# Performance work log

Measured on AMD Instinct MI355X. Metric: run time of the kernel, lower is better.

Reference implementation:

```python
import jax, jax.numpy as jnp
import numpy as np

B, T, C = 16, 2048, 64

def setup_inputs() -> dict:
    key = jax.random.key(0)
    x = jax.random.normal(key, (B, T, C), dtype=jnp.float32)
    # learned scalar params (as in build()): r_sigma init 0.01, margin init 0.0
    r_sigma = jnp.array([0.01], dtype=jnp.float32)
    margin = jnp.array([0.0], dtype=jnp.float32)
    return {"x": x, "r_sigma": r_sigma, "margin": margin}

def reference(x, r_sigma, margin):
    # Pairwise squared euclidean distances via the gram trick:
    # ||xi - xj||^2 = ||xi||^2 + ||xj||^2 - 2 xi.xj  (mathematically identical
    # to the original diff -> norm -> square, but avoids the (B,T,T,C) tensor
    # and the non-differentiable sqrt(0) on the diagonal).
    _, size, _ = x.shape
    sq = jnp.sum(x * x, axis=-1)                              # (B,T)
    gram = jnp.einsum('btc,bsc->bts', x, x)                   # (B,T,T)
    sqdist = jnp.maximum(sq[:, :, None] + sq[:, None, :] - 2.0 * gram, 0.0)
    # Gaussian kernel with learned inverse-bandwidth and margin
    Kmat = jnp.exp(-sqdist * r_sigma[0] + margin[0])          # (B,T,T)
    # off-diagonal mask (zero self-similarity)
    Kmat = Kmat * (1.0 - jnp.eye(size, dtype=x.dtype))
    # residual kernel attention: x + K @ x
    return x + jnp.einsum('bts,bsc->btc', Kmat, x)
```

## Files before the change

### kernel.cpp

```cpp
#include <hip/hip_runtime.h>
#include <stdint.h>
#include <stddef.h>

#define BB 16
#define TT 2048
#define CC 64

typedef __attribute__((ext_vector_type(8))) short short8;
typedef __attribute__((ext_vector_type(4))) float f32x4;

#if defined(__has_builtin)
#if __has_builtin(__builtin_amdgcn_exp2f)
#define EXP2(x) __builtin_amdgcn_exp2f(x)
#else
#define EXP2(x) exp2f(x)
#endif
#else
#define EXP2(x) exp2f(x)
#endif

static __device__ __forceinline__ unsigned short f2bf(float f) {
  union { float f; unsigned int u; } v; v.f = f;
  unsigned int u = v.u;
  return (unsigned short)((u + 0x7FFFu + ((u >> 16) & 1u)) >> 16);
}

__global__ __launch_bounds__(256) void prep_kernel(
    const float* __restrict__ x, unsigned short* __restrict__ xb,
    unsigned short* __restrict__ xbT, float* __restrict__ sq)
{
  __shared__ float tile[64][65];
  __shared__ float rs[64][4];
  const int b   = blockIdx.x >> 5;
  const int t0  = (blockIdx.x & 31) << 6;
  const int tid = threadIdx.x;
  const int r   = tid >> 2, qd = tid & 3;

  const float* src = x + ((size_t)(b * TT + t0 + r) * CC + qd * 16);
  float v[16];
  float ssq = 0.f;
#pragma unroll
  for (int k = 0; k < 4; ++k) {
    f32x4 t4 = ((const f32x4*)src)[k];
#pragma unroll
    for (int j = 0; j < 4; ++j) { float f = t4[j]; v[k * 4 + j] = f; ssq += f * f; }
  }

  unsigned short hb[16];
#pragma unroll
  for (int j = 0; j < 16; ++j) hb[j] = f2bf(v[j]);
  unsigned short* dstb = xb + ((size_t)(b * TT + t0 + r) * CC + qd * 16);
  ((short8*)dstb)[0] = *(const short8*)(hb);
  ((short8*)dstb)[1] = *(const short8*)(hb + 8);

#pragma unroll
  for (int j = 0; j < 16; ++j) tile[r][qd * 16 + j] = v[j];
  rs[r][qd] = ssq;
  __syncthreads();

  if (tid < 64)
    sq[(size_t)b * TT + t0 + tid] = rs[tid][0] + rs[tid][1] + rs[tid][2] + rs[tid][3];

  const int c = tid >> 2, tq = tid & 3;
  unsigned short ht[16];
#pragma unroll
  for (int j = 0; j < 16; ++j) ht[j] = f2bf(tile[tq * 16 + j][c]);
  unsigned short* dstT = xbT + ((size_t)(b * CC + c) * TT + t0 + tq * 16);
  ((short8*)dstT)[0] = *(const short8*)(ht);
  ((short8*)dstT)[1] = *(const short8*)(ht + 8);
}

__global__ __launch_bounds__(256, 2) void attn_kernel(
    const float* __restrict__ x, const unsigned short* __restrict__ xb,
    const unsigned short* __restrict__ xbT, const float* __restrict__ sq,
    const float* __restrict__ rsig, const float* __restrict__ marg,
    float* __restrict__ out)
{
  __shared__ unsigned short Klds[2][64 * 64];
  __shared__ unsigned short Vlds[2][64 * 64];
  __shared__ unsigned short Plds[4][16 * 64];

  const int bid = ((blockIdx.x & 7) << 6) | (blockIdx.x >> 3);
  const int b   = bid >> 5;
  const int qb  = (bid & 31) << 6;
  const int tid = threadIdx.x;
  const int w = tid >> 6, lane = tid & 63;
  const int hi = lane >> 4, lo = lane & 15;

  const float L2E = 1.44269504088896f;
  const float rl2 = -rsig[0] * L2E;
  const float ml2 = marg[0] * L2E;

  const unsigned short* xb_b  = xb  + (size_t)b * TT * CC;
  const unsigned short* xbT_b = xbT + (size_t)b * CC * TT;
  const float* sq_b = sq + (size_t)b * TT;

  const int q0 = qb + w * 16;

  short8 qf[2];
#pragma unroll
  for (int ks = 0; ks < 2; ++ks)
    qf[ks] = *(const short8*)(xb_b + (size_t)(q0 + lo) * CC + ks * 32 + hi * 8);

  float aq[4];
#pragma unroll
  for (int r = 0; r < 4; ++r) aq[r] = sq_b[q0 + hi * 4 + r];

  f32x4 oacc[4];
#pragma unroll
  for (int ct = 0; ct < 4; ++ct) oacc[ct] = (f32x4){0.f, 0.f, 0.f, 0.f};

  const int srow = tid >> 3, slot = tid & 7;
  const int swz0 = srow * 64        + ((slot ^ (srow & 7)) * 8);
  const int swz1 = (srow + 32) * 64 + ((slot ^ (srow & 7)) * 8);

  short8 stg0, stg1, stg2, stg3;

  auto LOADT = [&](int t) {
    const size_t sb = (size_t)t * 64;
    stg0 = *(const short8*)(xb_b  + (sb + srow) * CC + slot * 8);
    stg1 = *(const short8*)(xb_b  + (sb + 32 + srow) * CC + slot * 8);
    stg2 = *(const short8*)(xbT_b + (size_t)srow * TT + sb + slot * 8);
    stg3 = *(const short8*)(xbT_b + (size_t)(srow + 32) * TT + sb + slot * 8);
  };
  auto WRITET = [&](int bf) {
    *(short8*)(&Klds[bf][swz0]) = stg0;
    *(short8*)(&Klds[bf][swz1]) = stg1;
    *(short8*)(&Vlds[bf][swz0]) = stg2;
    *(short8*)(&Vlds[bf][swz1]) = stg3;
  };

  LOADT(0); WRITET(0);
  __syncthreads();

  for (int t = 0; t < 32; ++t) {
    const int cur = t & 1;
    if (t + 1 < 32) LOADT(t + 1);

    const int sb = t * 64;
    float as[4];
#pragma unroll
    for (int ct = 0; ct < 4; ++ct) as[ct] = sq_b[sb + ct * 16 + lo];

    f32x4 sac[4];
#pragma unroll
    for (int ct = 0; ct < 4; ++ct) sac[ct] = (f32x4){0.f, 0.f, 0.f, 0.f};

#pragma unroll
    for (int ct = 0; ct < 4; ++ct) {
#pragma unroll
      for (int ks = 0; ks < 2; ++ks) {
        const short8 kf = *(const short8*)(
            &Klds[cur][(ct * 16 + lo) * 64 + (((ks * 4 + hi) ^ (lo & 7)) * 8)]);
        sac[ct] = __builtin_amdgcn_mfma_f32_16x16x32_bf16(qf[ks], kf, sac[ct], 0, 0, 0);
      }
    }

    const bool dtile = (sb <= q0 + 15) && (q0 <= sb + 63);
#pragma unroll
    for (int ct = 0; ct < 4; ++ct) {
#pragma unroll
      for (int r = 0; r < 4; ++r) {
        float d = aq[r] + as[ct] - 2.f * sac[ct][r];
        d = fmaxf(d, 0.f);
        float kk = EXP2(fmaf(d, rl2, ml2));
        if (dtile && (q0 + hi * 4 + r == sb + ct * 16 + lo)) kk = 0.f;
        const int s = ct * 16 + lo, q = hi * 4 + r;
        Plds[w][q * 64 + (((s >> 3) ^ (q & 7)) * 8) + (s & 7)] = f2bf(kk);
      }
    }

    short8 pf[2];
#pragma unroll
    for (int ks = 0; ks < 2; ++ks)
      pf[ks] = *(const short8*)(
          &Plds[w][lo * 64 + (((ks * 4 + hi) ^ (lo & 7)) * 8)]);

#pragma unroll
    for (int ct = 0; ct < 4; ++ct) {
#pragma unroll
      for (int ks = 0; ks < 2; ++ks) {
        const short8 vf = *(const short8*)(
            &Vlds[cur][(ct * 16 + lo) * 64 + (((ks * 4 + hi) ^ (lo & 7)) * 8)]);
        oacc[ct] = __builtin_amdgcn_mfma_f32_16x16x32_bf16(pf[ks], vf, oacc[ct], 0, 0, 0);
      }
    }

    if (t + 1 < 32) WRITET(cur ^ 1);
    __syncthreads();
  }

#pragma unroll
  for (int ct = 0; ct < 4; ++ct) {
#pragma unroll
    for (int r = 0; r < 4; ++r) {
      const int q = q0 + hi * 4 + r;
      const int c = ct * 16 + lo;
      const size_t idx = (size_t)(b * TT + q) * CC + c;
      out[idx] = x[idx] + oacc[ct][r];
    }
  }
}

extern "C" void kernel_launch(void* const* d_in, const int* in_sizes, int n_in,
                              void* d_out, int out_size, void* d_ws, size_t ws_size,
                              hipStream_t stream) {
  const float* x    = (const float*)d_in[0];
  const float* rsig = (const float*)d_in[1];
  const float* marg = (const float*)d_in[2];
  float* out = (float*)d_out;

  unsigned short* xb  = (unsigned short*)d_ws;
  unsigned short* xbT = xb + (size_t)BB * TT * CC;
  float* sq = (float*)(xbT + (size_t)BB * TT * CC);

  prep_kernel<<<512, 256, 0, stream>>>(x, xb, xbT, sq);
  attn_kernel<<<512, 256, 0, stream>>>(x, xb, xbT, sq, rsig, marg, out);
}
```

Before: 111.0 us.

## Use 32x32 MFMA with register-resident P and split-K wave reduction

The attention kernel moves from 16x16x32 to 32x32x16 bf16 MFMA. Scores are computed transposed, so the P fragment can be packed directly in registers with v_cvt_pk_bf16 and v_permlane32_swap, with no LDS round trip. Waves are split into query halves and key halves, and partial outputs are reduced through LDS at the end. The prep kernel is also reworked into smaller 16-row blocks with a shuffle reduction and a bf16 LDS transpose, and it launches more blocks. The trade-off is extra LDS for the final reduction, plus inline asm that depends on gfx950 instructions.

```diff
diff --git a/kernel.cpp b/kernel.cpp
--- a/kernel.cpp
+++ b/kernel.cpp
@@ -7,7 +7,9 @@
 #define CC 64
 
 typedef __attribute__((ext_vector_type(8))) short short8;
+typedef __attribute__((ext_vector_type(4))) short s16x4;
 typedef __attribute__((ext_vector_type(4))) float f32x4;
+typedef __attribute__((ext_vector_type(16))) float f32x16;
 
 #if defined(__has_builtin)
 #if __has_builtin(__builtin_amdgcn_exp2f)
@@ -25,49 +27,53 @@
   return (unsigned short)((u + 0x7FFFu + ((u >> 16) & 1u)) >> 16);
 }
 
-__global__ __launch_bounds__(256) void prep_kernel(
+static __device__ __forceinline__ short8 pack_swap(
+    float a0, float a1, float a2, float a3,
+    float a4, float a5, float a6, float a7) {
+  unsigned X, Z, Y, W;
+  asm("v_cvt_pk_bf16_f32 %0, %1, %2" : "=v"(X) : "v"(a0), "v"(a1));
+  asm("v_cvt_pk_bf16_f32 %0, %1, %2" : "=v"(Z) : "v"(a2), "v"(a3));
+  asm("v_cvt_pk_bf16_f32 %0, %1, %2" : "=v"(Y) : "v"(a4), "v"(a5));
+  asm("v_cvt_pk_bf16_f32 %0, %1, %2" : "=v"(W) : "v"(a6), "v"(a7));
+  asm("v_permlane32_swap_b32 %0, %1" : "+v"(X), "+v"(Y));
+  asm("v_permlane32_swap_b32 %0, %1" : "+v"(Z), "+v"(W));
+  union { unsigned u[4]; short8 s; } u;
+  u.u[0] = X; u.u[1] = Z; u.u[2] = Y; u.u[3] = W;
+  return u.s;
+}
+
+__global__ __launch_bounds__(256, 4) void prep_kernel(
     const float* __restrict__ x, unsigned short* __restrict__ xb,
     unsigned short* __restrict__ xbT, float* __restrict__ sq)
 {
-  __shared__ float tile[64][65];
-  __shared__ float rs[64][4];
-  const int b   = blockIdx.x >> 5;
-  const int t0  = (blockIdx.x & 31) << 6;
+  __shared__ unsigned short tile[16 * 68];
+  const int b   = blockIdx.x >> 7;
+  const int t0  = (blockIdx.x & 127) << 4;
   const int tid = threadIdx.x;
-  const int r   = tid >> 2, qd = tid & 3;
-
-  const float* src = x + ((size_t)(b * TT + t0 + r) * CC + qd * 16);
-  float v[16];
-  float ssq = 0.f;
-#pragma unroll
-  for (int k = 0; k < 4; ++k) {
-    f32x4 t4 = ((const f32x4*)src)[k];
-#pragma unroll
-    for (int j = 0; j < 4; ++j) { float f = t4[j]; v[k * 4 + j] = f; ssq += f * f; }
-  }
-
-  unsigned short hb[16];
-#pragma unroll
-  for (int j = 0; j < 16; ++j) hb[j] = f2bf(v[j]);
-  unsigned short* dstb = xb + ((size_t)(b * TT + t0 + r) * CC + qd * 16);
-  ((short8*)dstb)[0] = *(const short8*)(hb);
-  ((short8*)dstb)[1] = *(const short8*)(hb + 8);
-
-#pragma unroll
-  for (int j = 0; j < 16; ++j) tile[r][qd * 16 + j] = v[j];
-  rs[r][qd] = ssq;
+  const int r   = tid >> 4;
+  const int cg  = tid & 15;
+  const int c4  = cg * 4;
+
+  const size_t idx = (size_t)(b * TT + t0 + r) * CC + c4;
+  const f32x4 v = *(const f32x4*)(x + idx);
+  float ssq = v[0]*v[0] + v[1]*v[1] + v[2]*v[2] + v[3]*v[3];
+
+  s16x4 hv;
+  hv[0] = (short)f2bf(v[0]); hv[1] = (short)f2bf(v[1]);
+  hv[2] = (short)f2bf(v[2]); hv[3] = (short)f2bf(v[3]);
+  *(s16x4*)(xb + idx) = hv;
+  *(s16x4*)(&tile[r * 68 + c4]) = hv;
+
+  ssq += __shfl_xor(ssq, 1); ssq += __shfl_xor(ssq, 2);
+  ssq += __shfl_xor(ssq, 4); ssq += __shfl_xor(ssq, 8);
+  if (cg == 0) sq[(size_t)b * TT + t0 + r] = ssq;
   __syncthreads();
 
-  if (tid < 64)
-    sq[(size_t)b * TT + t0 + tid] = rs[tid][0] + rs[tid][1] + rs[tid][2] + rs[tid][3];
-
   const int c = tid >> 2, tq = tid & 3;
-  unsigned short ht[16];
-#pragma unroll
-  for (int j = 0; j < 16; ++j) ht[j] = f2bf(tile[tq * 16 + j][c]);
-  unsigned short* dstT = xbT + ((size_t)(b * CC + c) * TT + t0 + tq * 16);
-  ((short8*)dstT)[0] = *(const short8*)(ht);
-  ((short8*)dstT)[1] = *(const short8*)(ht + 8);
+  s16x4 o;
+#pragma unroll
+  for (int k = 0; k < 4; ++k) o[k] = (short)tile[(tq * 4 + k) * 68 + c];
+  *(s16x4*)(xbT + (size_t)(b * CC + c) * TT + t0 + tq * 4) = o;
 }
 
 __global__ __launch_bounds__(256, 2) void attn_kernel(
@@ -78,14 +84,15 @@
 {
   __shared__ unsigned short Klds[2][64 * 64];
   __shared__ unsigned short Vlds[2][64 * 64];
-  __shared__ unsigned short Plds[4][16 * 64];
+  __shared__ float Red[2][32 * 64];
 
   const int bid = ((blockIdx.x & 7) << 6) | (blockIdx.x >> 3);
   const int b   = bid >> 5;
   const int qb  = (bid & 31) << 6;
   const int tid = threadIdx.x;
   const int w = tid >> 6, lane = tid & 63;
-  const int hi = lane >> 4, lo = lane & 15;
+  const int l31 = lane & 31, hi1 = lane >> 5;
+  const int wq = w & 1, ws = w >> 1;
 
   const float L2E = 1.44269504088896f;
   const float rl2 = -rsig[0] * L2E;
@@ -95,27 +102,25 @@
   const unsigned short* xbT_b = xbT + (size_t)b * CC * TT;
   const float* sq_b = sq + (size_t)b * TT;
 
-  const int q0 = qb + w * 16;
-
-  short8 qf[2];
-#pragma unroll
-  for (int ks = 0; ks < 2; ++ks)
-    qf[ks] = *(const short8*)(xb_b + (size_t)(q0 + lo) * CC + ks * 32 + hi * 8);
-
-  float aq[4];
-#pragma unroll
-  for (int r = 0; r < 4; ++r) aq[r] = sq_b[q0 + hi * 4 + r];
-
-  f32x4 oacc[4];
-#pragma unroll
-  for (int ct = 0; ct < 4; ++ct) oacc[ct] = (f32x4){0.f, 0.f, 0.f, 0.f};
+  const int q0w = qb + wq * 32;
+
+  short8 qf[4];
+#pragma unroll
+  for (int kc = 0; kc < 4; ++kc)
+    qf[kc] = *(const short8*)(xb_b + (size_t)(q0w + l31) * CC + kc * 16 + hi1 * 8);
+  const float aq = sq_b[q0w + l31];
+
+  f32x16 oacc[2];
+#pragma unroll
+  for (int ct = 0; ct < 2; ++ct)
+#pragma unroll
+    for (int i = 0; i < 16; ++i) oacc[ct][i] = 0.f;
 
   const int srow = tid >> 3, slot = tid & 7;
   const int swz0 = srow * 64        + ((slot ^ (srow & 7)) * 8);
   const int swz1 = (srow + 32) * 64 + ((slot ^ (srow & 7)) * 8);
 
   short8 stg0, stg1, stg2, stg3;
-
   auto LOADT = [&](int t) {
     const size_t sb = (size_t)t * 64;
     stg0 = *(const short8*)(xb_b  + (sb + srow) * CC + slot * 8);
@@ -133,56 +138,54 @@
   LOADT(0); WRITET(0);
   __syncthreads();
 
+  const int rr = ws * 32 + l31;
   for (int t = 0; t < 32; ++t) {
     const int cur = t & 1;
+    const int tb = t * 64;
     if (t + 1 < 32) LOADT(t + 1);
 
-    const int sb = t * 64;
-    float as[4];
-#pragma unroll
-    for (int ct = 0; ct < 4; ++ct) as[ct] = sq_b[sb + ct * 16 + lo];
-
-    f32x4 sac[4];
-#pragma unroll
-    for (int ct = 0; ct < 4; ++ct) sac[ct] = (f32x4){0.f, 0.f, 0.f, 0.f};
-
-#pragma unroll
-    for (int ct = 0; ct < 4; ++ct) {
-#pragma unroll
-      for (int ks = 0; ks < 2; ++ks) {
-        const short8 kf = *(const short8*)(
-            &Klds[cur][(ct * 16 + lo) * 64 + (((ks * 4 + hi) ^ (lo & 7)) * 8)]);
-        sac[ct] = __builtin_amdgcn_mfma_f32_16x16x32_bf16(qf[ks], kf, sac[ct], 0, 0, 0);
-      }
-    }
-
-    const bool dtile = (sb <= q0 + 15) && (q0 <= sb + 63);
-#pragma unroll
-    for (int ct = 0; ct < 4; ++ct) {
-#pragma unroll
-      for (int r = 0; r < 4; ++r) {
-        float d = aq[r] + as[ct] - 2.f * sac[ct][r];
-        d = fmaxf(d, 0.f);
-        float kk = EXP2(fmaf(d, rl2, ml2));
-        if (dtile && (q0 + hi * 4 + r == sb + ct * 16 + lo)) kk = 0.f;
-        const int s = ct * 16 + lo, q = hi * 4 + r;
-        Plds[w][q * 64 + (((s >> 3) ^ (q & 7)) * 8) + (s & 7)] = f2bf(kk);
-      }
-    }
-
-    short8 pf[2];
-#pragma unroll
-    for (int ks = 0; ks < 2; ++ks)
-      pf[ks] = *(const short8*)(
-          &Plds[w][lo * 64 + (((ks * 4 + hi) ^ (lo & 7)) * 8)]);
-
-#pragma unroll
-    for (int ct = 0; ct < 4; ++ct) {
-#pragma unroll
-      for (int ks = 0; ks < 2; ++ks) {
+    float aqas[16];
+#pragma unroll
+    for (int r = 0; r < 16; ++r)
+      aqas[r] = aq + sq_b[tb + ws * 32 + ((r & 3) + 8 * (r >> 2)) + 4 * hi1];
+
+    f32x16 sac;
+#pragma unroll
+    for (int i = 0; i < 16; ++i) sac[i] = 0.f;
+#pragma unroll
+    for (int kc = 0; kc < 4; ++kc) {
+      const short8 kf = *(const short8*)(
+          &Klds[cur][rr * 64 + (((kc * 2 + hi1) ^ (rr & 7)) * 8)]);
+      sac = __builtin_amdgcn_mfma_f32_32x32x16_bf16(kf, qf[kc], sac, 0, 0, 0);
+    }
+
+    float p[16];
+#pragma unroll
+    for (int r = 0; r < 16; ++r) {
+      float d = fmaf(sac[r], -2.f, aqas[r]);
+      d = fmaxf(d, 0.f);
+      p[r] = EXP2(fmaf(d, rl2, ml2));
+    }
+    if (tb + ws * 32 == qb + wq * 32) {
+#pragma unroll
+      for (int r = 0; r < 16; ++r) {
+        const int sl = (r & 3) + 8 * (r >> 2) + 4 * hi1;
+        if (sl == l31) p[r] = 0.f;
+      }
+    }
+
+    short8 af0 = pack_swap(p[0], p[1], p[2],  p[3],  p[4],  p[5],  p[6],  p[7]);
+    short8 af1 = pack_swap(p[8], p[9], p[10], p[11], p[12], p[13], p[14], p[15]);
+
+#pragma unroll
+    for (int ct = 0; ct < 2; ++ct) {
+      const int rowc = ct * 32 + l31;
+#pragma unroll
+      for (int kk = 0; kk < 2; ++kk) {
         const short8 vf = *(const short8*)(
-            &Vlds[cur][(ct * 16 + lo) * 64 + (((ks * 4 + hi) ^ (lo & 7)) * 8)]);
-        oacc[ct] = __builtin_amdgcn_mfma_f32_16x16x32_bf16(pf[ks], vf, oacc[ct], 0, 0, 0);
+            &Vlds[cur][rowc * 64 + (((ws * 4 + kk * 2 + hi1) ^ (rowc & 7)) * 8)]);
+        oacc[ct] = __builtin_amdgcn_mfma_f32_32x32x16_bf16(
+            kk ? af1 : af0, vf, oacc[ct], 0, 0, 0);
       }
     }
 
@@ -190,15 +193,26 @@
     __syncthreads();
   }
 
-#pragma unroll
-  for (int ct = 0; ct < 4; ++ct) {
-#pragma unroll
-    for (int r = 0; r < 4; ++r) {
-      const int q = q0 + hi * 4 + r;
-      const int c = ct * 16 + lo;
-      const size_t idx = (size_t)(b * TT + q) * CC + c;
-      out[idx] = x[idx] + oacc[ct][r];
-    }
+  if (ws == 1) {
+#pragma unroll
+    for (int ct = 0; ct < 2; ++ct)
+#pragma unroll
+      for (int r = 0; r < 16; ++r) {
+        const int ql = (r & 3) + 8 * (r >> 2) + 4 * hi1;
+        Red[wq][ql * 64 + ct * 32 + l31] = oacc[ct][r];
+      }
+  }
+  __syncthreads();
+  if (ws == 0) {
+#pragma unroll
+    for (int ct = 0; ct < 2; ++ct)
+#pragma unroll
+      for (int r = 0; r < 16; ++r) {
+        const int ql = (r & 3) + 8 * (r >> 2) + 4 * hi1;
+        const int c  = ct * 32 + l31;
+        const size_t idx = (size_t)(b * TT + qb + wq * 32 + ql) * CC + c;
+        out[idx] = x[idx] + oacc[ct][r] + Red[wq][ql * 64 + c];
+      }
   }
 }
 
@@ -214,6 +228,6 @@
   unsigned short* xbT = xb + (size_t)BB * TT * CC;
   float* sq = (float*)(xbT + (size_t)BB * TT * CC);
 
-  prep_kernel<<<512, 256, 0, stream>>>(x, xb, xbT, sq);
+  prep_kernel<<<2048, 256, 0, stream>>>(x, xb, xbT, sq);
   attn_kernel<<<512, 256, 0, stream>>>(x, xb, xbT, sq, rsig, marg, out);
 }
```

Measured after the change: 100.1 us. 1.11x faster.
